# Kernel optimization log

Measured on AMD Instinct MI355X. Metric: run time of the kernel, lower is better.

Reference implementation:

```python
import jax, jax.numpy as jnp
import numpy as np

N_NODES = 100000
N_EDGES = 800000


def setup_inputs() -> dict:
    key = jax.random.key(0)
    ks = jax.random.split(key, 8)
    s = 0.05  # weight scale
    return {
        "x": jax.random.normal(ks[0], (N_NODES, 64), dtype=jnp.float32),
        "edge_index": jax.random.randint(ks[1], (2, N_EDGES), 0, N_NODES, dtype=jnp.int64),
        "eps1": jnp.zeros((), jnp.float32),
        "eps2": jnp.zeros((), jnp.float32),
        "W1a": jax.random.normal(ks[2], (64, 128), dtype=jnp.float32) * s,
        "b1a": jnp.zeros((128,), jnp.float32),
        "W1b": jax.random.normal(ks[3], (128, 128), dtype=jnp.float32) * s,
        "b1b": jnp.zeros((128,), jnp.float32),
        "W2a": jax.random.normal(ks[4], (128, 128), dtype=jnp.float32) * s,
        "b2a": jnp.zeros((128,), jnp.float32),
        "W2b": jax.random.normal(ks[5], (128, 64), dtype=jnp.float32) * s,
        "b2b": jnp.zeros((64,), jnp.float32),
    }


def _gin_conv(h, src, dst, eps, Wa, ba, Wb, bb, n_nodes):
    # sum-aggregate neighbor messages h[src] at dst, add (1+eps)*self
    agg = jax.ops.segment_sum(h[src], dst, num_segments=n_nodes)  # [N, d]
    z = (1.0 + eps) * h + agg
    # MLP: Linear -> ReLU -> Linear (weights stored [in, out])
    return jnp.maximum(z @ Wa + ba, 0.0) @ Wb + bb


def reference(x, edge_index, eps1, eps2, W1a, b1a, W1b, b1b, W2a, b2a, W2b, b2b):
    src, dst = edge_index[0], edge_index[1]
    n = x.shape[0]
    h = _gin_conv(x, src, dst, eps1, W1a, b1a, W1b, b1b, n)
    h = jnp.maximum(h, 0.0)  # outer ReLU; dropout is identity in eval
    out = _gin_conv(h, src, dst, eps2, W2a, b2a, W2b, b2b, n)
    return out
```

## Files before the change

kernel.cpp:

```cpp
#include <hip/hip_runtime.h>
#include <cstdint>

constexpr int CAP = 32;
constexpr int CAPA = 16;
constexpr int FIX = 16;

typedef __attribute__((ext_vector_type(8))) __bf16 bf16x8;
typedef __attribute__((ext_vector_type(16))) float f32x16;
typedef _Float16 f16x2 __attribute__((ext_vector_type(2)));

__device__ __forceinline__ unsigned short f2bf(float f) {
    unsigned int u = __builtin_bit_cast(unsigned int, f);
    u += 0x7fffu + ((u >> 16) & 1u);
    return (unsigned short)(u >> 16);
}
__device__ __forceinline__ float bf2f(unsigned short h) {
    unsigned int u = ((unsigned int)h) << 16;
    return __builtin_bit_cast(float, u);
}
__device__ __forceinline__ unsigned short f2h(float f) {
    _Float16 h = (_Float16)f;
    return __builtin_bit_cast(unsigned short, h);
}
__device__ __forceinline__ float h2f(unsigned short u) {
    return (float)__builtin_bit_cast(_Float16, u);
}
__device__ __forceinline__ float2 h2f2(unsigned int u) {
    f16x2 h = __builtin_bit_cast(f16x2, u);
    return make_float2((float)h.x, (float)h.y);
}


__global__ void zero_kernel(int* __restrict__ p, int n) {
    int i = blockIdx.x * 256 + threadIdx.x;
    if (i < n) p[i] = 0;
}


__global__ void build_kernel(const int* __restrict__ eidx, int E,
                             int* __restrict__ counts, int* __restrict__ bktA,
                             int* __restrict__ bktB,
                             const float* __restrict__ W1a, const float* __restrict__ W1b,
                             const float* __restrict__ W2a, const float* __restrict__ W2b,
                             unsigned short* __restrict__ wpk,
                             const float* __restrict__ x, unsigned short* __restrict__ xf16,
                             int N) {
    const int i = blockIdx.x * 256 + threadIdx.x;
    const int stride = gridDim.x * 256;

    for (int e = i; e < E; e += stride) {
        int s = eidx[e];
        int d = eidx[E + e];
        int pos = atomicAdd(&counts[d], 1);
        if (pos < CAPA) {
            bktA[(unsigned int)d * 16u + pos] = s;
        } else if (pos < CAP) {
            bktB[(unsigned int)d * 16u + (pos - CAPA)] = s;
        }
    }

    if (i < 49152) {
        const float* W;
        int K, Nn, base, rel;
        if (i < 8192) {
            W = W1a; K = 64; Nn = 128; base = 0; rel = i;
        } else if (i < 24576) {
            W = W1b; K = 128; Nn = 128; base = 16384; rel = i - 8192;
        } else if (i < 40960) {
            W = W2a; K = 128; Nn = 128; base = 49152; rel = i - 24576;
        } else {
            W = W2b; K = 128; Nn = 64; base = 81920; rel = i - 40960;
        }
        int j = rel & 7;
        int lane = (rel >> 3) & 63;
        int rest = rel >> 9;
        int ksteps = K / 16;
        int kstep = rest % ksteps;
        int ntile = rest / ksteps;
        int k = kstep * 16 + ((lane >> 5) << 3) + j;
        int ncol = ntile * 32 + (lane & 31);
        float v = W[k * Nn + ncol];
        unsigned short h = f2bf(v);
        unsigned short l = f2bf(v - bf2f(h));
        wpk[base + rel] = h;
        wpk[base + K * Nn + rel] = l;
    }

    const int total4 = N * 16;
    for (int t = i; t < total4; t += stride) {
        float4 v = ((const float4*)x)[t];
        ushort4 o;
        o.x = f2h(v.x);
        o.y = f2h(v.y);
        o.z = f2h(v.z);
        o.w = f2h(v.w);
        ((ushort4*)xf16)[t] = o;
    }
}


template <int KIN, int KMID, int KOUT, bool RELU_OUT, bool SELF_F32, bool F16_OUT>
__global__ __launch_bounds__(256, 8) void gin_layer_kernel(
    const unsigned short* __restrict__ gf16, const float* __restrict__ hf32,
    const int* __restrict__ cnts,
    const int* __restrict__ bktA, const int* __restrict__ bktB,
    const float* __restrict__ eps,
    const unsigned short* __restrict__ Wahi, const unsigned short* __restrict__ Walo,
    const float* __restrict__ ba,
    const unsigned short* __restrict__ Wbhi, const unsigned short* __restrict__ Wblo,
    const float* __restrict__ bb, float* __restrict__ out_f32,
    unsigned short* __restrict__ outf16, int n) {
    constexpr int ZS = KIN + 8;
    constexpr int TS = KMID + 8;
    constexpr int KSB = KIN / 16;
    constexpr int KSC = KMID / 16;
    __shared__ __align__(16) unsigned short smem[2 * 32 * (KMID + 8)];
    unsigned short* const zhi = smem;
    unsigned short* const zlo = smem + 32 * ZS;
    unsigned short* const thi = smem;
    unsigned short* const tlo = smem + 32 * TS;

    const int tid = threadIdx.x;
    const int lane = tid & 63;
    const int base = blockIdx.x * 32;
    const float scale = 1.0f + eps[0];
    const int wq = __builtin_amdgcn_readfirstlane(tid >> 6);

    float h0x, h0y;
    if (KIN == 64) {
        h0x = h2f(gf16[lane]);
        h0y = 0.f;
    } else {
        float2 t0 = h2f2(((const unsigned int*)gf16)[lane]);
        h0x = t0.x;
        h0y = t0.y;
    }

#pragma unroll
    for (int mi = 0; mi < 8; ++mi) {
        const int m = wq * 8 + mi;
        const int node = base + m;
        const int nc = node < n ? node : n - 1;
        const int cl0 = __builtin_amdgcn_readfirstlane(cnts[nc]);
        const int cl = cl0 < CAP ? cl0 : CAP;
        const int* __restrict__ srcs = bktA + (unsigned int)nc * 16u;

        int sIdx[FIX];
#pragma unroll
        for (int j = 0; j < FIX; ++j) {
            int sj = srcs[j];
            sIdx[j] = j < cl ? sj : 0;
        }

        if (KIN == 64) {
            float a0 = 0.f, a1 = 0.f, a2 = 0.f, a3 = 0.f;
            float a4 = 0.f, a5 = 0.f, a6 = 0.f, a7 = 0.f;
#pragma unroll
            for (int j = 0; j < FIX; j += 8) {
                a0 += h2f(gf16[(unsigned int)sIdx[j + 0] * 64u + lane]);
                a1 += h2f(gf16[(unsigned int)sIdx[j + 1] * 64u + lane]);
                a2 += h2f(gf16[(unsigned int)sIdx[j + 2] * 64u + lane]);
                a3 += h2f(gf16[(unsigned int)sIdx[j + 3] * 64u + lane]);
                a4 += h2f(gf16[(unsigned int)sIdx[j + 4] * 64u + lane]);
                a5 += h2f(gf16[(unsigned int)sIdx[j + 5] * 64u + lane]);
                a6 += h2f(gf16[(unsigned int)sIdx[j + 6] * 64u + lane]);
                a7 += h2f(gf16[(unsigned int)sIdx[j + 7] * 64u + lane]);
            }
            float self;
            if (SELF_F32) {
                self = hf32[(unsigned int)nc * 64u + lane];
            } else {
                self = h2f(gf16[(unsigned int)nc * 64u + lane]);
            }
            float res = scale * self;
            res += ((a0 + a1) + (a2 + a3)) + ((a4 + a5) + (a6 + a7));
            float corr = (float)(FIX - (cl < FIX ? cl : FIX));
            res = __builtin_fmaf(-corr, h0x, res);
            for (int e = FIX; e < cl; ++e)
                res += h2f(gf16[(unsigned int)bktB[(unsigned int)nc * 16u + (e - FIX)] * 64u +
                               lane]);
            unsigned short rh = f2bf(res);
            zhi[m * ZS + lane] = rh;
            zlo[m * ZS + lane] = f2bf(res - bf2f(rh));
        } else {
            const unsigned int* g32 = (const unsigned int*)gf16;
            float x0 = 0.f, x1 = 0.f, x2 = 0.f, x3 = 0.f;
            float y0 = 0.f, y1 = 0.f, y2 = 0.f, y3 = 0.f;
#pragma unroll
            for (int j = 0; j < FIX; j += 4) {
                float2 v0 = h2f2(g32[(unsigned int)sIdx[j + 0] * 64u + lane]);
                float2 v1 = h2f2(g32[(unsigned int)sIdx[j + 1] * 64u + lane]);
                float2 v2 = h2f2(g32[(unsigned int)sIdx[j + 2] * 64u + lane]);
                float2 v3 = h2f2(g32[(unsigned int)sIdx[j + 3] * 64u + lane]);
                x0 += v0.x;
                y0 += v0.y;
                x1 += v1.x;
                y1 += v1.y;
                x2 += v2.x;
                y2 += v2.y;
                x3 += v3.x;
                y3 += v3.y;
            }
            float sx, sy;
            if (SELF_F32) {
                const float2* h2 = (const float2*)hf32;
                float2 a = h2[(unsigned int)nc * 64u + lane];
                sx = a.x;
                sy = a.y;
            } else {
                float2 a = h2f2(g32[(unsigned int)nc * 64u + lane]);
                sx = a.x;
                sy = a.y;
            }
            float ax = scale * sx + ((x0 + x1) + (x2 + x3));
            float ay = scale * sy + ((y0 + y1) + (y2 + y3));
            float corr = (float)(FIX - (cl < FIX ? cl : FIX));
            ax = __builtin_fmaf(-corr, h0x, ax);
            ay = __builtin_fmaf(-corr, h0y, ay);
            for (int e = FIX; e < cl; ++e) {
                float2 v =
                    h2f2(g32[(unsigned int)bktB[(unsigned int)nc * 16u + (e - FIX)] * 64u + lane]);
                ax += v.x;
                ay += v.y;
            }
            unsigned short hx = f2bf(ax), hy = f2bf(ay);
            unsigned short lx = f2bf(ax - bf2f(hx)), ly = f2bf(ay - bf2f(hy));
            *(unsigned int*)(zhi + m * ZS + 2 * lane) = (unsigned int)hx | ((unsigned int)hy << 16);
            *(unsigned int*)(zlo + m * ZS + 2 * lane) = (unsigned int)lx | ((unsigned int)ly << 16);
        }
    }
    __syncthreads();

    const int r31 = lane & 31;
    const int q = lane >> 5;

    {
        const int nt = wq;
        f32x16 acc;
#pragma unroll
        for (int i = 0; i < 16; ++i) acc[i] = 0.0f;
        const unsigned short* Ah = zhi + r31 * ZS + q * 8;
        const unsigned short* Al = zlo + r31 * ZS + q * 8;
        const unsigned short* Bh = Wahi + ((size_t)(nt * KSB) * 64 + lane) * 8;
        const unsigned short* Bl = Walo + ((size_t)(nt * KSB) * 64 + lane) * 8;
#pragma unroll
        for (int ks = 0; ks < KSB; ++ks) {
            bf16x8 ah = *reinterpret_cast<const bf16x8*>(Ah + ks * 16);
            bf16x8 al = *reinterpret_cast<const bf16x8*>(Al + ks * 16);
            bf16x8 bh = *reinterpret_cast<const bf16x8*>(Bh + ks * 512);
            bf16x8 bl = *reinterpret_cast<const bf16x8*>(Bl + ks * 512);
            acc = __builtin_amdgcn_mfma_f32_32x32x16_bf16(ah, bh, acc, 0, 0, 0);
            acc = __builtin_amdgcn_mfma_f32_32x32x16_bf16(ah, bl, acc, 0, 0, 0);
            acc = __builtin_amdgcn_mfma_f32_32x32x16_bf16(al, bh, acc, 0, 0, 0);
        }
        const int col = nt * 32 + r31;
        const float bias = ba[col];
        unsigned short th_r[16], tl_r[16];
#pragma unroll
        for (int i = 0; i < 16; ++i) {
            float v = fmaxf(acc[i] + bias, 0.0f);
            unsigned short hh = f2bf(v);
            th_r[i] = hh;
            tl_r[i] = f2bf(v - bf2f(hh));
        }
        __syncthreads();
#pragma unroll
        for (int i = 0; i < 16; ++i) {
            const int m = (i & 3) + 8 * (i >> 2) + 4 * q;
            thi[m * TS + col] = th_r[i];
            tlo[m * TS + col] = tl_r[i];
        }
    }
    __syncthreads();

    {
        constexpr int NKS = (KOUT == 64) ? (KSC / 2) : KSC;
        const int nt = (KOUT == 64) ? (wq & 1) : wq;
        const int k0 = (KOUT == 64) ? ((wq >> 1) * NKS) : 0;
        f32x16 acc;
#pragma unroll
        for (int i = 0; i < 16; ++i) acc[i] = 0.0f;
        const unsigned short* Ah = thi + r31 * TS + q * 8 + k0 * 16;
        const unsigned short* Al = tlo + r31 * TS + q * 8 + k0 * 16;
        const unsigned short* Bh = Wbhi + ((size_t)(nt * KSC + k0) * 64 + lane) * 8;
        const unsigned short* Bl = Wblo + ((size_t)(nt * KSC + k0) * 64 + lane) * 8;
#pragma unroll
        for (int ks = 0; ks < NKS; ++ks) {
            bf16x8 ah = *reinterpret_cast<const bf16x8*>(Ah + ks * 16);
            bf16x8 al = *reinterpret_cast<const bf16x8*>(Al + ks * 16);
            bf16x8 bh = *reinterpret_cast<const bf16x8*>(Bh + ks * 512);
            bf16x8 bl = *reinterpret_cast<const bf16x8*>(Bl + ks * 512);
            acc = __builtin_amdgcn_mfma_f32_32x32x16_bf16(ah, bh, acc, 0, 0, 0);
            acc = __builtin_amdgcn_mfma_f32_32x32x16_bf16(ah, bl, acc, 0, 0, 0);
            acc = __builtin_amdgcn_mfma_f32_32x32x16_bf16(al, bh, acc, 0, 0, 0);
        }
        const int col = nt * 32 + r31;
        if (KOUT == 64) {
            __syncthreads();
            float* stg = (float*)smem;
            if (wq >= 2) {
                float* d = stg + ((wq - 2) * 64 + lane) * 20;
#pragma unroll
                for (int c = 0; c < 4; ++c) {
                    float4 v = make_float4(acc[4 * c + 0], acc[4 * c + 1], acc[4 * c + 2],
                                           acc[4 * c + 3]);
                    *reinterpret_cast<float4*>(d + c * 4) = v;
                }
            }
            __syncthreads();
            if (wq < 2) {
                const float* s = stg + (wq * 64 + lane) * 20;
#pragma unroll
                for (int i = 0; i < 16; ++i) acc[i] += s[i];
                const float bias = bb[col];
#pragma unroll
                for (int i = 0; i < 16; ++i) {
                    const int m = (i & 3) + 8 * (i >> 2) + 4 * q;
                    const int node = base + m;
                    if (node < n) {
                        float v = acc[i] + bias;
                        if (RELU_OUT) v = fmaxf(v, 0.0f);
                        out_f32[(size_t)node * KOUT + col] = v;
                    }
                }
            }
        } else {
            const float bias = bb[col];
#pragma unroll
            for (int i = 0; i < 16; ++i) {
                const int m = (i & 3) + 8 * (i >> 2) + 4 * q;
                const int node = base + m;
                if (node < n) {
                    float v = acc[i] + bias;
                    if (RELU_OUT) v = fmaxf(v, 0.0f);
                    if (F16_OUT) {
                        outf16[(size_t)node * KOUT + col] = f2h(v);
                    } else {
                        out_f32[(size_t)node * KOUT + col] = v;
                    }
                }
            }
        }
    }
}


extern "C" void kernel_launch(void* const* d_in, const int* in_sizes, int n_in,
                              void* d_out, int out_size, void* d_ws, size_t ws_size,
                              hipStream_t stream) {
    const float* x = (const float*)d_in[0];
    const int* eidx = (const int*)d_in[1];
    const float* eps1 = (const float*)d_in[2];
    const float* eps2 = (const float*)d_in[3];
    const float* W1a = (const float*)d_in[4];
    const float* b1a = (const float*)d_in[5];
    const float* W1b = (const float*)d_in[6];
    const float* b1b = (const float*)d_in[7];
    const float* W2a = (const float*)d_in[8];
    const float* b2a = (const float*)d_in[9];
    const float* W2b = (const float*)d_in[10];
    const float* b2b = (const float*)d_in[11];
    float* out = (float*)d_out;

    int N = in_sizes[0] / 64;
    int E = in_sizes[1] / 2;

    char* p = (char*)d_ws;
    auto alloc = [&](size_t bytes) {
        char* r = p;
        p += (bytes + 255) & ~(size_t)255;
        return r;
    };
    int* counts = (int*)alloc((size_t)N * 4);
    int* bktA = (int*)alloc((size_t)N * CAPA * 4);
    int* bktB = (int*)alloc((size_t)N * CAPA * 4);
    unsigned short* h1f = (unsigned short*)alloc((size_t)N * 128 * 2);
    unsigned short* xf16 = (unsigned short*)alloc((size_t)N * 64 * 2);
    unsigned short* wpk = (unsigned short*)alloc(98304 * 2);

    int zb = (N + 255) / 256;
    int eb = (E + 255) / 256;
    int gb = (N + 31) / 32;

    zero_kernel<<<zb, 256, 0, stream>>>(counts, N);
    build_kernel<<<eb, 256, 0, stream>>>(eidx, E, counts, bktA, bktB, W1a, W1b, W2a, W2b, wpk, x,
                                         xf16, N);

    gin_layer_kernel<64, 128, 128, true, true, true><<<gb, 256, 0, stream>>>(
        xf16, x, counts, bktA, bktB, eps1, wpk + 0, wpk + 8192, b1a, wpk + 16384, wpk + 32768, b1b,
        (float*)nullptr, h1f, N);
    gin_layer_kernel<128, 128, 64, false, false, false><<<gb, 256, 0, stream>>>(
        h1f, (const float*)nullptr, counts, bktA, bktB, eps2, wpk + 49152, wpk + 65536, b2a,
        wpk + 81920, wpk + 90112, b2b, out, (unsigned short*)nullptr, N);
}
```

Baseline: 220.8 us.

## Partition edge bucketing by XCD and accumulate gathers in packed fp16

```diff
diff --git a/kernel.cpp b/kernel.cpp
--- a/kernel.cpp
+++ b/kernel.cpp
@@ -4,6 +4,8 @@
 constexpr int CAP = 32;
 constexpr int CAPA = 16;
 constexpr int FIX = 16;
+constexpr int CH = 2048;
+constexpr int NXCD = 8;
 
 typedef __attribute__((ext_vector_type(8))) __bf16 bf16x8;
 typedef __attribute__((ext_vector_type(16))) float f32x16;
@@ -29,6 +31,11 @@
     f16x2 h = __builtin_bit_cast(f16x2, u);
     return make_float2((float)h.x, (float)h.y);
 }
+__device__ __forceinline__ int get_xcd() {
+    int x;
+    asm volatile("s_getreg_b32 %0, hwreg(HW_REG_XCC_ID)" : "=s"(x));
+    return x & (NXCD - 1);
+}
 
 
 __global__ void zero_kernel(int* __restrict__ p, int n) {
@@ -37,39 +44,42 @@
 }
 
 
+__device__ __forceinline__ void push_edge(int d, int s, int lo, int ns,
+                                          int* __restrict__ counts, int* __restrict__ bktA,
+                                          int* __restrict__ bktB) {
+    if ((unsigned)(d - lo) < (unsigned)ns) {
+        int pos = atomicAdd(&counts[d], 1);
+        if (pos < CAPA) {
+            bktA[(unsigned int)d * 16u + pos] = s;
+        } else if (pos < CAP) {
+            bktB[(unsigned int)d * 16u + (pos - CAPA)] = s;
+        }
+    }
+}
+
 __global__ void build_kernel(const int* __restrict__ eidx, int E,
-                             int* __restrict__ counts, int* __restrict__ bktA,
-                             int* __restrict__ bktB,
+                             int* __restrict__ counts, int* __restrict__ tickets,
+                             int* __restrict__ bktA, int* __restrict__ bktB,
                              const float* __restrict__ W1a, const float* __restrict__ W1b,
                              const float* __restrict__ W2a, const float* __restrict__ W2b,
                              unsigned short* __restrict__ wpk,
                              const float* __restrict__ x, unsigned short* __restrict__ xf16,
                              int N) {
-    const int i = blockIdx.x * 256 + threadIdx.x;
+    const int tid = threadIdx.x;
+    const int gi = blockIdx.x * 256 + tid;
     const int stride = gridDim.x * 256;
 
-    for (int e = i; e < E; e += stride) {
-        int s = eidx[e];
-        int d = eidx[E + e];
-        int pos = atomicAdd(&counts[d], 1);
-        if (pos < CAPA) {
-            bktA[(unsigned int)d * 16u + pos] = s;
-        } else if (pos < CAP) {
-            bktB[(unsigned int)d * 16u + (pos - CAPA)] = s;
-        }
-    }
-
-    if (i < 49152) {
+    if (gi < 49152) {
         const float* W;
         int K, Nn, base, rel;
-        if (i < 8192) {
-            W = W1a; K = 64; Nn = 128; base = 0; rel = i;
-        } else if (i < 24576) {
-            W = W1b; K = 128; Nn = 128; base = 16384; rel = i - 8192;
-        } else if (i < 40960) {
-            W = W2a; K = 128; Nn = 128; base = 49152; rel = i - 24576;
+        if (gi < 8192) {
+            W = W1a; K = 64; Nn = 128; base = 0; rel = gi;
+        } else if (gi < 24576) {
+            W = W1b; K = 128; Nn = 128; base = 16384; rel = gi - 8192;
+        } else if (gi < 40960) {
+            W = W2a; K = 128; Nn = 128; base = 49152; rel = gi - 24576;
         } else {
-            W = W2b; K = 128; Nn = 64; base = 81920; rel = i - 40960;
+            W = W2b; K = 128; Nn = 64; base = 81920; rel = gi - 40960;
         }
         int j = rel & 7;
         int lane = (rel >> 3) & 63;
@@ -87,7 +97,7 @@
     }
 
     const int total4 = N * 16;
-    for (int t = i; t < total4; t += stride) {
+    for (int t = gi; t < total4; t += stride) {
         float4 v = ((const float4*)x)[t];
         ushort4 o;
         o.x = f2h(v.x);
@@ -95,6 +105,39 @@
         o.z = f2h(v.z);
         o.w = f2h(v.w);
         ((ushort4*)xf16)[t] = o;
+    }
+
+    const int xcd = get_xcd();
+    const int ns = (N + NXCD - 1) / NXCD;
+    const int lo = xcd * ns;
+    const int nchunk = (E + CH - 1) / CH;
+    __shared__ int s_chunk;
+    for (;;) {
+        if (tid == 0) s_chunk = atomicAdd(&tickets[xcd], 1);
+        __syncthreads();
+        const int c = s_chunk;
+        __syncthreads();
+        if (c >= nchunk) break;
+        const int e0 = c * CH + tid * 8;
+        if (e0 + 7 < E) {
+            int4 da = *(const int4*)(eidx + E + e0);
+            int4 db = *(const int4*)(eidx + E + e0 + 4);
+            int4 sa = *(const int4*)(eidx + e0);
+            int4 sb = *(const int4*)(eidx + e0 + 4);
+            push_edge(da.x, sa.x, lo, ns, counts, bktA, bktB);
+            push_edge(da.y, sa.y, lo, ns, counts, bktA, bktB);
+            push_edge(da.z, sa.z, lo, ns, counts, bktA, bktB);
+            push_edge(da.w, sa.w, lo, ns, counts, bktA, bktB);
+            push_edge(db.x, sb.x, lo, ns, counts, bktA, bktB);
+            push_edge(db.y, sb.y, lo, ns, counts, bktA, bktB);
+            push_edge(db.z, sb.z, lo, ns, counts, bktA, bktB);
+            push_edge(db.w, sb.w, lo, ns, counts, bktA, bktB);
+        } else {
+            for (int j = 0; j < 8; ++j) {
+                int e = e0 + j;
+                if (e < E) push_edge(eidx[E + e], eidx[e], lo, ns, counts, bktA, bktB);
+            }
+        }
     }
 }
 
@@ -153,18 +196,13 @@
         }
 
         if (KIN == 64) {
-            float a0 = 0.f, a1 = 0.f, a2 = 0.f, a3 = 0.f;
-            float a4 = 0.f, a5 = 0.f, a6 = 0.f, a7 = 0.f;
-#pragma unroll
-            for (int j = 0; j < FIX; j += 8) {
-                a0 += h2f(gf16[(unsigned int)sIdx[j + 0] * 64u + lane]);
-                a1 += h2f(gf16[(unsigned int)sIdx[j + 1] * 64u + lane]);
-                a2 += h2f(gf16[(unsigned int)sIdx[j + 2] * 64u + lane]);
-                a3 += h2f(gf16[(unsigned int)sIdx[j + 3] * 64u + lane]);
-                a4 += h2f(gf16[(unsigned int)sIdx[j + 4] * 64u + lane]);
-                a5 += h2f(gf16[(unsigned int)sIdx[j + 5] * 64u + lane]);
-                a6 += h2f(gf16[(unsigned int)sIdx[j + 6] * 64u + lane]);
-                a7 += h2f(gf16[(unsigned int)sIdx[j + 7] * 64u + lane]);
+            _Float16 p0 = (_Float16)0, p1 = (_Float16)0, p2 = (_Float16)0, p3 = (_Float16)0;
+#pragma unroll
+            for (int j = 0; j < FIX; j += 4) {
+                p0 += __builtin_bit_cast(_Float16, gf16[(unsigned int)sIdx[j + 0] * 64u + lane]);
+                p1 += __builtin_bit_cast(_Float16, gf16[(unsigned int)sIdx[j + 1] * 64u + lane]);
+                p2 += __builtin_bit_cast(_Float16, gf16[(unsigned int)sIdx[j + 2] * 64u + lane]);
+                p3 += __builtin_bit_cast(_Float16, gf16[(unsigned int)sIdx[j + 3] * 64u + lane]);
             }
             float self;
             if (SELF_F32) {
@@ -173,7 +211,7 @@
                 self = h2f(gf16[(unsigned int)nc * 64u + lane]);
             }
             float res = scale * self;
-            res += ((a0 + a1) + (a2 + a3)) + ((a4 + a5) + (a6 + a7));
+            res += (((float)p0 + (float)p1) + ((float)p2 + (float)p3));
             float corr = (float)(FIX - (cl < FIX ? cl : FIX));
             res = __builtin_fmaf(-corr, h0x, res);
             for (int e = FIX; e < cl; ++e)
@@ -184,22 +222,14 @@
             zlo[m * ZS + lane] = f2bf(res - bf2f(rh));
         } else {
             const unsigned int* g32 = (const unsigned int*)gf16;
-            float x0 = 0.f, x1 = 0.f, x2 = 0.f, x3 = 0.f;
-            float y0 = 0.f, y1 = 0.f, y2 = 0.f, y3 = 0.f;
+            f16x2 q0 = {(_Float16)0, (_Float16)0};
+            f16x2 q1 = q0, q2 = q0, q3 = q0;
 #pragma unroll
             for (int j = 0; j < FIX; j += 4) {
-                float2 v0 = h2f2(g32[(unsigned int)sIdx[j + 0] * 64u + lane]);
-                float2 v1 = h2f2(g32[(unsigned int)sIdx[j + 1] * 64u + lane]);
-                float2 v2 = h2f2(g32[(unsigned int)sIdx[j + 2] * 64u + lane]);
-                float2 v3 = h2f2(g32[(unsigned int)sIdx[j + 3] * 64u + lane]);
-                x0 += v0.x;
-                y0 += v0.y;
-                x1 += v1.x;
-                y1 += v1.y;
-                x2 += v2.x;
-                y2 += v2.y;
-                x3 += v3.x;
-                y3 += v3.y;
+                q0 += __builtin_bit_cast(f16x2, g32[(unsigned int)sIdx[j + 0] * 64u + lane]);
+                q1 += __builtin_bit_cast(f16x2, g32[(unsigned int)sIdx[j + 1] * 64u + lane]);
+                q2 += __builtin_bit_cast(f16x2, g32[(unsigned int)sIdx[j + 2] * 64u + lane]);
+                q3 += __builtin_bit_cast(f16x2, g32[(unsigned int)sIdx[j + 3] * 64u + lane]);
             }
             float sx, sy;
             if (SELF_F32) {
@@ -212,8 +242,8 @@
                 sx = a.x;
                 sy = a.y;
             }
-            float ax = scale * sx + ((x0 + x1) + (x2 + x3));
-            float ay = scale * sy + ((y0 + y1) + (y2 + y3));
+            float ax = scale * sx + (((float)q0.x + (float)q1.x) + ((float)q2.x + (float)q3.x));
+            float ay = scale * sy + (((float)q0.y + (float)q1.y) + ((float)q2.y + (float)q3.y));
             float corr = (float)(FIX - (cl < FIX ? cl : FIX));
             ax = __builtin_fmaf(-corr, h0x, ax);
             ay = __builtin_fmaf(-corr, h0y, ay);
@@ -371,20 +401,21 @@
         p += (bytes + 255) & ~(size_t)255;
         return r;
     };
-    int* counts = (int*)alloc((size_t)N * 4);
+    int* counts = (int*)alloc((size_t)(N + NXCD) * 4);
+    int* tickets = counts + N;
     int* bktA = (int*)alloc((size_t)N * CAPA * 4);
     int* bktB = (int*)alloc((size_t)N * CAPA * 4);
     unsigned short* h1f = (unsigned short*)alloc((size_t)N * 128 * 2);
     unsigned short* xf16 = (unsigned short*)alloc((size_t)N * 64 * 2);
     unsigned short* wpk = (unsigned short*)alloc(98304 * 2);
 
-    int zb = (N + 255) / 256;
+    int zb = (N + NXCD + 255) / 256;
     int eb = (E + 255) / 256;
     int gb = (N + 31) / 32;
 
-    zero_kernel<<<zb, 256, 0, stream>>>(counts, N);
-    build_kernel<<<eb, 256, 0, stream>>>(eidx, E, counts, bktA, bktB, W1a, W1b, W2a, W2b, wpk, x,
-                                         xf16, N);
+    zero_kernel<<<zb, 256, 0, stream>>>(counts, N + NXCD);
+    build_kernel<<<eb, 256, 0, stream>>>(eidx, E, counts, tickets, bktA, bktB, W1a, W1b, W2a, W2b,
+                                         wpk, x, xf16, N);
 
     gin_layer_kernel<64, 128, 128, true, true, true><<<gb, 256, 0, stream>>>(
         xf16, x, counts, bktA, bktB, eps1, wpk + 0, wpk + 8192, b1a, wpk + 16384, wpk + 32768, b1b,
```

New measurement: 269.3 us. +22.0%, slower.
